# Kernel tuning notes

Hardware: AMD Instinct MI355X
Metric: run time of the kernel (lower is better)

Reference implementation:

```python
import jax, jax.numpy as jnp
import numpy as np


def setup_inputs() -> dict:
    key = jax.random.key(0)
    ks = jax.random.split(key, 5)
    B, C, H, W = 4, 64, 64, 64
    C8 = C // 8
    return {
        "x_opt": jax.random.normal(ks[0], (B, C, H, W), jnp.float32),
        "x_sar": jax.random.normal(ks[1], (B, C, H, W), jnp.float32),
        "wq": jax.random.normal(ks[2], (C8, C), jnp.float32) * 0.05,
        "bq": jnp.zeros((C8,), jnp.float32),
        "wk": jax.random.normal(ks[3], (C8, C), jnp.float32) * 0.05,
        "bk": jnp.zeros((C8,), jnp.float32),
        "wv": jax.random.normal(ks[4], (C, C), jnp.float32) * 0.05,
        "bv": jnp.zeros((C,), jnp.float32),
        "gamma": jnp.zeros((1,), jnp.float32),
    }


def reference(x_opt, x_sar, wq, bq, wk, bk, wv, bv, gamma):
    b, c, h, w = x_opt.shape
    n = h * w
    xo = x_opt.reshape(b, c, n)  # [b, c, N]
    xs = x_sar.reshape(b, c, n)
    # 1x1 convs == channel matmuls
    q = jnp.einsum('oc,bcn->bon', wq, xo) + bq[None, :, None]  # [b, c//8, N]
    k = jnp.einsum('oc,bcn->bon', wk, xs) + bk[None, :, None]  # [b, c//8, N]
    v = jnp.einsum('oc,bcn->bon', wv, xs) + bv[None, :, None]  # [b, c, N]
    # attn[b, n, m] = softmax_m( q[:, :, n] . k[:, :, m] )  -- NO 1/sqrt(d) scaling
    scores = jnp.einsum('bdn,bdm->bnm', q, k)  # [b, N, N]
    attn = jax.nn.softmax(scores, axis=-1)
    # out[b, c, n] = sum_m v[b, c, m] * attn[b, n, m]
    out = jnp.einsum('bcm,bnm->bcn', v, attn).reshape(b, c, h, w)
    return gamma[0] * out + x_opt
```

## Files before the change

kernel.cpp:

```cpp
#include <hip/hip_runtime.h>
#include <hip/hip_bf16.h>
#include <stdint.h>

#define NDIM 4096
#define CDIM 64
#define NSPLIT 8
#define SPAN (NDIM / NSPLIT)
#define KBLK 128
#define NIT (SPAN / KBLK)
#define NQ4 (SPAN / 32)
#define LOG2E 1.44269504088896f

typedef float f32x16 __attribute__((ext_vector_type(16)));
typedef short bf16x8 __attribute__((ext_vector_type(8)));
union U4B { uint4 u; bf16x8 b; };

static __device__ __forceinline__ uint32_t cvtpk(float lo, float hi) {
  uint32_t r;
  asm("v_cvt_pk_bf16_f32 %0, %1, %2" : "=v"(r) : "v"(lo), "v"(hi));
  return r;
}
static __device__ __forceinline__ uint16_t f2bf(float f) {
  uint32_t r;
  asm("v_cvt_pk_bf16_f32 %0, %1, %1" : "=v"(r) : "v"(f));
  return (uint16_t)r;
}
static __device__ __forceinline__ float fexp2(float x) {
  return __builtin_amdgcn_exp2f(x);
}
static __device__ __forceinline__ void gload_lds16(const void* g, void* l) {
  __builtin_amdgcn_global_load_lds(
      (const __attribute__((address_space(1))) uint32_t*)g,
      (__attribute__((address_space(3))) uint32_t*)l, 16, 0, 0);
}

__global__ __launch_bounds__(256) void proj_kernel(
    const float* __restrict__ x_opt, const float* __restrict__ x_sar,
    const float* __restrict__ wq, const float* __restrict__ bq,
    const float* __restrict__ wk, const float* __restrict__ bk,
    const float* __restrict__ wvp, const float* __restrict__ bv,
    uint16_t* __restrict__ qf, uint16_t* __restrict__ kf,
    uint16_t* __restrict__ vf)
{
  const int tid = threadIdx.x;
  const int w = tid >> 6;
  const int l = tid & 63;
  const int x = l & 31;
  const int hi = l >> 5;
  const int cg = w >> 1;
  const int half = w & 1;

  const int id = blockIdx.x;
  const int b = id >> 6;
  const int n0 = (id & 63) * 64 + cg * 32;
  const size_t xbase = (size_t)b * CDIM * NDIM;

  bf16x8 xsB[4];
#pragma unroll
  for (int kc = 0; kc < 4; kc++) {
    float sv[8];
#pragma unroll
    for (int j = 0; j < 8; j++)
      sv[j] = x_sar[xbase + (size_t)(kc * 16 + hi * 8 + j) * NDIM + n0 + x];
    U4B us;
    us.u = make_uint4(cvtpk(sv[0], sv[1]), cvtpk(sv[2], sv[3]),
                      cvtpk(sv[4], sv[5]), cvtpk(sv[6], sv[7]));
    xsB[kc] = us.b;
  }

  bf16x8 vA[4];
#pragma unroll
  for (int kc = 0; kc < 4; kc++) {
    const float* wr = wvp + (half * 32 + x) * 64 + kc * 16 + hi * 8;
    float4 wa = ((const float4*)wr)[0];
    float4 wb = ((const float4*)wr)[1];
    U4B u;
    u.u = make_uint4(cvtpk(wa.x, wa.y), cvtpk(wa.z, wa.w),
                     cvtpk(wb.x, wb.y), cvtpk(wb.z, wb.w));
    vA[kc] = u.b;
  }

  const f32x16 z16 = {0.f,0.f,0.f,0.f, 0.f,0.f,0.f,0.f,
                      0.f,0.f,0.f,0.f, 0.f,0.f,0.f,0.f};
  f32x16 aV = z16;
#pragma unroll
  for (int kc = 0; kc < 4; kc++)
    aV = __builtin_amdgcn_mfma_f32_32x32x16_bf16(vA[kc], xsB[kc], aV, 0, 0, 0);
#pragma unroll
  for (int r = 0; r < 16; r++) {
    const int row = half * 32 + (r & 3) + 8 * (r >> 2) + 4 * hi;
    vf[(size_t)(b * 64 + row) * NDIM + n0 + x] = f2bf(aV[r] + bv[row]);
  }

  bf16x8 gA[4], gB[4];
#pragma unroll
  for (int kc = 0; kc < 4; kc++) {
    U4B ua;
    ua.u = make_uint4(0u, 0u, 0u, 0u);
    if (x < 8) {
      const float* wr = (half ? wk : wq) + x * 64 + kc * 16 + hi * 8;
      float4 wa = ((const float4*)wr)[0];
      float4 wb = ((const float4*)wr)[1];
      ua.u = make_uint4(cvtpk(wa.x, wa.y), cvtpk(wa.z, wa.w),
                        cvtpk(wb.x, wb.y), cvtpk(wb.z, wb.w));
    }
    gA[kc] = ua.b;
    if (half == 0) {
      float ov[8];
#pragma unroll
      for (int j = 0; j < 8; j++)
        ov[j] = x_opt[xbase + (size_t)(kc * 16 + hi * 8 + j) * NDIM + n0 + x];
      U4B uo;
      uo.u = make_uint4(cvtpk(ov[0], ov[1]), cvtpk(ov[2], ov[3]),
                        cvtpk(ov[4], ov[5]), cvtpk(ov[6], ov[7]));
      gB[kc] = uo.b;
    } else {
      gB[kc] = xsB[kc];
    }
  }
  f32x16 aG = z16;
#pragma unroll
  for (int kc = 0; kc < 4; kc++)
    aG = __builtin_amdgcn_mfma_f32_32x32x16_bf16(gA[kc], gB[kc], aG, 0, 0, 0);

  const float* bias = half ? bk : bq;
  const float scl = half ? 1.0f : LOG2E;
  float gv[4];
#pragma unroll
  for (int r = 0; r < 4; r++) gv[r] = (aG[r] + bias[4 * hi + r]) * scl;
  uint16_t* dst = half ? kf : qf;
  const size_t nrow = ((size_t)b * NDIM + n0 + x) * 16;
  uint2 st;
  st.x = cvtpk(gv[0], gv[1]); st.y = cvtpk(gv[2], gv[3]);
  *(uint2*)(dst + nrow + hi * 4) = st;
  if (hi == 0) {
    const uint4 z4 = make_uint4(0u, 0u, 0u, 0u);
    *(uint4*)(dst + nrow + 8) = z4;
  }
}

__global__ __launch_bounds__(256, 4) void attn_kernel(
    const uint16_t* __restrict__ qf, const uint16_t* __restrict__ kf,
    const uint16_t* __restrict__ vf,
    uint16_t* __restrict__ po, float* __restrict__ ls)
{
  __shared__ __align__(16) uint16_t vt[2][64][128];

  const int tid = threadIdx.x;
  const int w = tid >> 6;
  const int l = tid & 63;
  const int x = l & 31;
  const int hi = l >> 5;

  const int id = blockIdx.x;
  const int sp = id & 7;
  const int qb = (id >> 3) & 31;
  const int b = id >> 8;

  const int n0 = qb * 128;
  const uint16_t* vsrc = vf + (size_t)b * CDIM * NDIM + sp * SPAN;
  const uint16_t* ksrc = kf + ((size_t)b * NDIM + sp * SPAN) * 16;
  const int qrow = n0 + w * 32 + x;

  U4B qfr;
  qfr.u = *(const uint4*)(qf + ((size_t)b * NDIM + qrow) * 16 + hi * 8);

  uint32_t voff[16];
#pragma unroll
  for (int k = 0; k < 16; k++) voff[k] = (uint32_t)((k ^ (x & 15)) << 4);

  const f32x16 z16 = {0.f,0.f,0.f,0.f, 0.f,0.f,0.f,0.f,
                      0.f,0.f,0.f,0.f, 0.f,0.f,0.f,0.f};
  f32x16 oacc0 = z16, oacc1 = z16;
  float lacc[4] = {0.f, 0.f, 0.f, 0.f};

  auto stageV = [&](int t, int buf) {
#pragma unroll
    for (int si = 0; si < 4; si++) {
      const int rowbase = w * 16 + si * 4;
      const int row = rowbase + (l >> 4);
      gload_lds16(vsrc + (size_t)row * NDIM + t * KBLK +
                      (((l & 15) ^ (row & 15)) << 3),
                  &vt[buf][rowbase][0]);
    }
  };

  stageV(0, 0);
  uint4 kcur = *(const uint4*)(ksrc + (size_t)x * 16 + hi * 8);
  __syncthreads();

  for (int it = 0; it < NIT; it++) {
    const int cur = it & 1;
    if (it + 1 < NIT) stageV(it + 1, cur ^ 1);
    const uint8_t* vb = (const uint8_t*)&vt[cur][0][0];
    const uint8_t* vrow0 = vb + (size_t)x * 256;
    const uint8_t* vrow1 = vb + (size_t)(32 + x) * 256;

#pragma unroll
    for (int q4 = 0; q4 < 4; q4++) {
      const int gq = it * 4 + q4;
      uint4 knx = *(const uint4*)(ksrc + ((size_t)(gq + 1) * 32 + x) * 16 + hi * 8);

      U4B ka; ka.u = kcur;
      f32x16 s = __builtin_amdgcn_mfma_f32_32x32x16_bf16(ka.b, qfr.b, z16, 0, 0, 0);

      float p[16];
#pragma unroll
      for (int i = 0; i < 16; i++) p[i] = fexp2(s[i]);
      float t8[8];
#pragma unroll
      for (int i = 0; i < 8; i++) t8[i] = p[i] + p[i + 8];
#pragma unroll
      for (int i = 0; i < 4; i++) lacc[i] += t8[i] + t8[i + 4];

      uint32_t W[8];
#pragma unroll
      for (int j = 0; j < 8; j++) W[j] = cvtpk(p[2 * j], p[2 * j + 1]);

      __builtin_amdgcn_s_setprio(1);
#pragma unroll
      for (int sub = 0; sub < 2; sub++) {
        uint32_t a0 = W[sub * 4 + 0], b0 = W[sub * 4 + 2];
        uint32_t a1 = W[sub * 4 + 1], b1 = W[sub * 4 + 3];
        asm("v_permlane32_swap_b32 %0, %1" : "+v"(a0), "+v"(b0));
        asm("v_permlane32_swap_b32 %0, %1" : "+v"(a1), "+v"(b1));
        U4B pf;
        pf.u = make_uint4(a0, a1, b0, b1);
        const int k = (q4 * 2 + sub) * 2 + hi;
        (void)k;
        const int kbase = (q4 * 2 + sub) * 2;
        U4B vf0, vf1;
        vf0.u = *(const uint4*)(vrow0 + voff[kbase + hi]);
        vf1.u = *(const uint4*)(vrow1 + voff[kbase + hi]);
        oacc0 = __builtin_amdgcn_mfma_f32_32x32x16_bf16(vf0.b, pf.b, oacc0, 0, 0, 0);
        oacc1 = __builtin_amdgcn_mfma_f32_32x32x16_bf16(vf1.b, pf.b, oacc1, 0, 0, 0);
      }
      __builtin_amdgcn_s_setprio(0);
      kcur = knx;
    }
    __syncthreads();
  }

  uint16_t* prow = po + (((size_t)sp * 4 + b) * NDIM + qrow) * CDIM;
#pragma unroll
  for (int cb = 0; cb < 2; cb++) {
    const f32x16 oa = (cb == 0) ? oacc0 : oacc1;
#pragma unroll
    for (int u = 0; u < 4; u++) {
      uint2 st;
      st.x = cvtpk(oa[u * 4 + 0], oa[u * 4 + 1]);
      st.y = cvtpk(oa[u * 4 + 2], oa[u * 4 + 3]);
      *(uint2*)(prow + cb * 32 + u * 8 + hi * 4) = st;
    }
  }
  float ltot = (lacc[0] + lacc[1]) + (lacc[2] + lacc[3]);
  ltot += __shfl_xor(ltot, 32);
  if (hi == 0)
    ls[((size_t)sp * 4 + b) * NDIM + qrow] = ltot;
}

__global__ __launch_bounds__(256) void merge_kernel(
    const uint16_t* __restrict__ po, const float* __restrict__ ls,
    const float* __restrict__ x_opt, const float* __restrict__ gamma,
    float* __restrict__ out)
{
  __shared__ float ot[32][65];
  const int tid = threadIdx.x;
  const int b = blockIdx.x >> 7;
  const int n0 = (blockIdx.x & 127) * 32;
  {
    const int q = tid >> 3;
    const int co = (tid & 7) * 8;
    const int nq = n0 + q;
    float wsum = 0.f;
    float acc[8] = {0.f, 0.f, 0.f, 0.f, 0.f, 0.f, 0.f, 0.f};
#pragma unroll
    for (int s = 0; s < NSPLIT; s++) {
      wsum += ls[((size_t)s * 4 + b) * NDIM + nq];
      const uint4 pv = *(const uint4*)(po + (((size_t)s * 4 + b) * NDIM + nq) * CDIM + co);
      const uint32_t* pw = (const uint32_t*)&pv;
#pragma unroll
      for (int j = 0; j < 4; j++) {
        acc[j * 2 + 0] += __uint_as_float(pw[j] << 16);
        acc[j * 2 + 1] += __uint_as_float(pw[j] & 0xFFFF0000u);
      }
    }
    const float inv = 1.f / wsum;
#pragma unroll
    for (int j = 0; j < 8; j++) ot[q][co + j] = acc[j] * inv;
  }
  __syncthreads();
  {
    const float gm = gamma[0];
    const int c = tid >> 2;
    const int j8 = (tid & 3) * 8;
    const float* xp = x_opt + ((size_t)b * CDIM + c) * NDIM + n0 + j8;
    float* op = out + ((size_t)b * CDIM + c) * NDIM + n0 + j8;
#pragma unroll
    for (int h = 0; h < 2; h++) {
      float4 xv = ((const float4*)xp)[h];
      float4 ov;
      ov.x = gm * ot[j8 + h * 4 + 0][c] + xv.x;
      ov.y = gm * ot[j8 + h * 4 + 1][c] + xv.y;
      ov.z = gm * ot[j8 + h * 4 + 2][c] + xv.z;
      ov.w = gm * ot[j8 + h * 4 + 3][c] + xv.w;
      ((float4*)op)[h] = ov;
    }
  }
}

extern "C" void kernel_launch(void* const* d_in, const int* in_sizes, int n_in,
                              void* d_out, int out_size, void* d_ws, size_t ws_size,
                              hipStream_t stream) {
  const float* x_opt = (const float*)d_in[0];
  const float* x_sar = (const float*)d_in[1];
  const float* wq    = (const float*)d_in[2];
  const float* bq    = (const float*)d_in[3];
  const float* wk    = (const float*)d_in[4];
  const float* bk    = (const float*)d_in[5];
  const float* wvp   = (const float*)d_in[6];
  const float* bv    = (const float*)d_in[7];
  const float* gamma = (const float*)d_in[8];
  float* outp = (float*)d_out;

  uint16_t* qf = (uint16_t*)d_ws;
  uint16_t* kf = (uint16_t*)((char*)d_ws + 524288);
  uint16_t* vf = (uint16_t*)((char*)d_ws + 1048576);
  uint16_t* po = (uint16_t*)((char*)d_ws + 3145728);
  float* lsp   = (float*)((char*)d_ws + 19922944);

  proj_kernel<<<256, 256, 0, stream>>>(x_opt, x_sar, wq, bq, wk, bk, wvp, bv,
                                       qf, kf, vf);
  attn_kernel<<<1024, 256, 0, stream>>>(qf, kf, vf, po, lsp);
  merge_kernel<<<512, 256, 0, stream>>>(po, lsp, x_opt, gamma, outp);
}
```

Before: 39.22 us.

## Software-pipeline QK MFMA one step ahead of exp and PV in attention loop

Flattens the attention loop into a single fully unrolled 16-step loop. Each step issues the next step's score MFMA before the exp, convert and PV work on the current scores, with K fragments prefetched two steps ahead. The per-lane swizzled V offset table is replaced by a base pointer plus XOR arithmetic, and launch bounds drop from 4 to 3 waves per EU so the extra live accumulators fit in registers. The aim is to hide MFMA and exp latency, at the cost of more registers and possibly lower occupancy.

```diff
diff --git a/kernel.cpp b/kernel.cpp
--- a/kernel.cpp
+++ b/kernel.cpp
@@ -8,7 +8,6 @@
 #define SPAN (NDIM / NSPLIT)
 #define KBLK 128
 #define NIT (SPAN / KBLK)
-#define NQ4 (SPAN / 32)
 #define LOG2E 1.44269504088896f
 
 typedef float f32x16 __attribute__((ext_vector_type(16)));
@@ -139,7 +138,7 @@
   }
 }
 
-__global__ __launch_bounds__(256, 4) void attn_kernel(
+__global__ __launch_bounds__(256, 3) void attn_kernel(
     const uint16_t* __restrict__ qf, const uint16_t* __restrict__ kf,
     const uint16_t* __restrict__ vf,
     uint16_t* __restrict__ po, float* __restrict__ ls)
@@ -165,9 +164,9 @@
   U4B qfr;
   qfr.u = *(const uint4*)(qf + ((size_t)b * NDIM + qrow) * 16 + hi * 8);
 
-  uint32_t voff[16];
-#pragma unroll
-  for (int k = 0; k < 16; k++) voff[k] = (uint32_t)((k ^ (x & 15)) << 4);
+  const uint32_t xh4 = (uint32_t)(((x & 15) ^ hi) << 4);
+  const uint8_t* vbase0 = (const uint8_t*)&vt[0][0][0] + (size_t)x * 256 + xh4;
+  const uint8_t* vbase1 = vbase0 + 16384;
 
   const f32x16 z16 = {0.f,0.f,0.f,0.f, 0.f,0.f,0.f,0.f,
                       0.f,0.f,0.f,0.f, 0.f,0.f,0.f,0.f};
@@ -186,59 +185,61 @@
   };
 
   stageV(0, 0);
-  uint4 kcur = *(const uint4*)(ksrc + (size_t)x * 16 + hi * 8);
+  uint4 kc = *(const uint4*)(ksrc + (size_t)x * 16 + hi * 8);
   __syncthreads();
-
-  for (int it = 0; it < NIT; it++) {
-    const int cur = it & 1;
-    if (it + 1 < NIT) stageV(it + 1, cur ^ 1);
-    const uint8_t* vb = (const uint8_t*)&vt[cur][0][0];
-    const uint8_t* vrow0 = vb + (size_t)x * 256;
-    const uint8_t* vrow1 = vb + (size_t)(32 + x) * 256;
-
-#pragma unroll
-    for (int q4 = 0; q4 < 4; q4++) {
-      const int gq = it * 4 + q4;
-      uint4 knx = *(const uint4*)(ksrc + ((size_t)(gq + 1) * 32 + x) * 16 + hi * 8);
-
-      U4B ka; ka.u = kcur;
-      f32x16 s = __builtin_amdgcn_mfma_f32_32x32x16_bf16(ka.b, qfr.b, z16, 0, 0, 0);
-
-      float p[16];
-#pragma unroll
-      for (int i = 0; i < 16; i++) p[i] = fexp2(s[i]);
-      float t8[8];
-#pragma unroll
-      for (int i = 0; i < 8; i++) t8[i] = p[i] + p[i + 8];
-#pragma unroll
-      for (int i = 0; i < 4; i++) lacc[i] += t8[i] + t8[i + 4];
-
-      uint32_t W[8];
-#pragma unroll
-      for (int j = 0; j < 8; j++) W[j] = cvtpk(p[2 * j], p[2 * j + 1]);
-
-      __builtin_amdgcn_s_setprio(1);
-#pragma unroll
-      for (int sub = 0; sub < 2; sub++) {
-        uint32_t a0 = W[sub * 4 + 0], b0 = W[sub * 4 + 2];
-        uint32_t a1 = W[sub * 4 + 1], b1 = W[sub * 4 + 3];
-        asm("v_permlane32_swap_b32 %0, %1" : "+v"(a0), "+v"(b0));
-        asm("v_permlane32_swap_b32 %0, %1" : "+v"(a1), "+v"(b1));
-        U4B pf;
-        pf.u = make_uint4(a0, a1, b0, b1);
-        const int k = (q4 * 2 + sub) * 2 + hi;
-        (void)k;
-        const int kbase = (q4 * 2 + sub) * 2;
-        U4B vf0, vf1;
-        vf0.u = *(const uint4*)(vrow0 + voff[kbase + hi]);
-        vf1.u = *(const uint4*)(vrow1 + voff[kbase + hi]);
-        oacc0 = __builtin_amdgcn_mfma_f32_32x32x16_bf16(vf0.b, pf.b, oacc0, 0, 0, 0);
-        oacc1 = __builtin_amdgcn_mfma_f32_32x32x16_bf16(vf1.b, pf.b, oacc1, 0, 0, 0);
-      }
-      __builtin_amdgcn_s_setprio(0);
-      kcur = knx;
-    }
-    __syncthreads();
+  uint4 kn = *(const uint4*)(ksrc + ((size_t)32 + x) * 16 + hi * 8);
+  U4B ka; ka.u = kc;
+  f32x16 scur = __builtin_amdgcn_mfma_f32_32x32x16_bf16(ka.b, qfr.b, z16, 0, 0, 0);
+  kc = kn;
+
+#pragma unroll
+  for (int gq = 0; gq < 16; gq++) {
+    const int it = gq >> 2;
+    const int q4 = gq & 3;
+
+    if (q4 == 0 && it + 1 < NIT) stageV(it + 1, (it + 1) & 1);
+
+    uint4 kn2 = *(const uint4*)(ksrc + ((size_t)(gq + 2) * 32 + x) * 16 + hi * 8);
+
+    U4B kb; kb.u = kc;
+    f32x16 snxt = __builtin_amdgcn_mfma_f32_32x32x16_bf16(kb.b, qfr.b, z16, 0, 0, 0);
+    kc = kn2;
+
+    float p[16];
+#pragma unroll
+    for (int i = 0; i < 16; i++) p[i] = fexp2(scur[i]);
+    float t8[8];
+#pragma unroll
+    for (int i = 0; i < 8; i++) t8[i] = p[i] + p[i + 8];
+#pragma unroll
+    for (int i = 0; i < 4; i++) lacc[i] += t8[i] + t8[i + 4];
+
+    uint32_t W[8];
+#pragma unroll
+    for (int j = 0; j < 8; j++) W[j] = cvtpk(p[2 * j], p[2 * j + 1]);
+
+    const uint8_t* vb = (it & 1) ? vbase1 : vbase0;
+    __builtin_amdgcn_s_setprio(1);
+#pragma unroll
+    for (int sub = 0; sub < 2; sub++) {
+      uint32_t a0 = W[sub * 4 + 0], b0 = W[sub * 4 + 2];
+      uint32_t a1 = W[sub * 4 + 1], b1 = W[sub * 4 + 3];
+      asm("v_permlane32_swap_b32 %0, %1" : "+v"(a0), "+v"(b0));
+      asm("v_permlane32_swap_b32 %0, %1" : "+v"(a1), "+v"(b1));
+      U4B pf;
+      pf.u = make_uint4(a0, a1, b0, b1);
+      const uint32_t kb4 = (uint32_t)((q4 * 4 + sub * 2) << 4);
+      const uint8_t* va = vb + (kb4 ^ xh4) - xh4;
+      U4B vf0, vf1;
+      vf0.u = *(const uint4*)(va);
+      vf1.u = *(const uint4*)(va + 8192);
+      oacc0 = __builtin_amdgcn_mfma_f32_32x32x16_bf16(vf0.b, pf.b, oacc0, 0, 0, 0);
+      oacc1 = __builtin_amdgcn_mfma_f32_32x32x16_bf16(vf1.b, pf.b, oacc1, 0, 0, 0);
+    }
+    __builtin_amdgcn_s_setprio(0);
+
+    if (q4 == 3) __syncthreads();
+    scur = snxt;
   }
 
   uint16_t* prow = po + (((size_t)sp * 4 + b) * NDIM + qrow) * CDIM;
```

Result: faster. 38.21 us (-2.6%).
